# Kernel tuning notes

Hardware: AMD Instinct MI355X
Metric: run time of the kernel (lower is better)

## Reference

```python
import jax, jax.numpy as jnp
import numpy as np

N_CODES = 512
CODE_DIM = 32
BETA = 0.25


def setup_inputs() -> dict:
    key = jax.random.key(0)
    k1, k2 = jax.random.split(key)
    z_e = jax.random.normal(k1, (8192, 64, CODE_DIM), dtype=jnp.float32)
    # codebook initialized uniform in [-1/n_codes, 1/n_codes] as in the torch module
    codebook = jax.random.uniform(
        k2, (N_CODES, CODE_DIM), dtype=jnp.float32,
        minval=-1.0 / N_CODES, maxval=1.0 / N_CODES)
    return {"z_e": z_e, "codebook": codebook}


def reference(z_e, codebook):
    # squared-distance matrix: ||z||^2 - 2 z.W^T + ||W||^2  -> [B, T, n_codes]
    dists = (jnp.sum(z_e * z_e, axis=-1, keepdims=True)
             - 2.0 * jnp.einsum('btd,nd->btn', z_e, codebook)
             + jnp.sum(codebook * codebook, axis=-1))
    indices = jnp.argmin(dists, axis=-1)          # [B, T] int
    z_q = codebook[indices]                        # [B, T, code_dim]
    sg = jax.lax.stop_gradient
    codebook_loss = jnp.mean((z_q - sg(z_e)) ** 2)
    commit_loss = jnp.mean((z_e - sg(z_q)) ** 2)
    loss = codebook_loss + BETA * commit_loss
    # straight-through estimator
    z_q_st = z_e + sg(z_q - z_e)
    return (z_q_st, indices, loss)
```

## Files before the change

### kernel.cpp

```cpp
#include <hip/hip_runtime.h>

#define N_CODES 512
#define D 32
#define NVEC (8192 * 64)
#define ZQ_ELEMS (NVEC * D)
#define BT 512
#define NBLK (NVEC / BT)
#define MARGIN_TRIG 7e-5f
#define SA (-1.0f / 16.0f)
#define SB (32.0f)
#define KMASK5 0xFFFFFFE0u

typedef _Float16 half8 __attribute__((ext_vector_type(8)));
typedef float f32x4 __attribute__((ext_vector_type(4)));

#define WW1_OFF 2112
#define BFRAG_OFF 4160
#define WT_OFF 36928
#define PART_OFF 102464
#define WL_OFF 118848
#define STAGE_F4 2176

__device__ __forceinline__ unsigned umin_(unsigned a, unsigned b) { return a < b ? a : b; }
__device__ __forceinline__ unsigned umax_(unsigned a, unsigned b) { return a > b ? a : b; }

__global__ void vq_prep(const float* __restrict__ cb, float* __restrict__ ww,
                        float* __restrict__ ww1, half8* __restrict__ bfrag,
                        float* __restrict__ wT, unsigned* __restrict__ flagcnt) {
    int gid = blockIdx.x * 256 + threadIdx.x;
    if (gid == 0) *flagcnt = 0u;
    {
        int flat = gid * 4;
        int d = flat >> 9, c = flat & 511;
        float4 v;
        v.x = cb[(size_t)(c + 0) * D + d];
        v.y = cb[(size_t)(c + 1) * D + d];
        v.z = cb[(size_t)(c + 2) * D + d];
        v.w = cb[(size_t)(c + 3) * D + d];
        *(float4*)(wT + flat) = v;
    }
    if (gid < 2048) {
        int t = gid >> 6, l = gid & 63;
        int code = t * 16 + (l & 15), koff = (l >> 4) * 8;
        const float* w = cb + (size_t)code * D + koff;
        half8 h;
#pragma unroll
        for (int j = 0; j < 8; ++j) h[j] = (_Float16)(SB * w[j]);
        bfrag[t * 64 + l] = h;
    }
    if (gid < N_CODES) {
        const float* wr = cb + (size_t)gid * D;
        double s = 0.0;
#pragma unroll
        for (int d = 0; d < D; ++d) s = fma((double)wr[d], (double)wr[d], s);
        ww[gid] = (float)s;
        ww1[gid] = (float)(1.0 + s);
    }
}

__global__ __launch_bounds__(BT, 6) void vq_main(
        const float* __restrict__ z, const float* __restrict__ cbf,
        const float4* __restrict__ stage_src,
        float* __restrict__ zq, float* __restrict__ idxo,
        double* __restrict__ partials, unsigned* __restrict__ flagcnt,
        int* __restrict__ worklist, int wl_cap) {
    __shared__ __align__(16) char smem[43008];
    __shared__ double wsum[8];
    const int tid = threadIdx.x;

    {
        float4* s4 = (float4*)smem;
#pragma unroll
        for (int i = 0; i < 5; ++i) {
            int k = i * BT + tid;
            if (k < STAGE_F4) s4[k] = stage_src[k];
        }
    }
    const float* lds_cin = (const float*)smem;
    const char* lds_bf = smem + 2048;
    float4* scratch = (float4*)(smem + 34816);

    const int l = tid & 63, wv = tid >> 6;
    const int g16 = l & 15, kg = l >> 4, koff = kg * 8;
    const int vblock = blockIdx.x * BT;
    const int vwave = vblock + wv * 64;

    __syncthreads();

#pragma unroll 1
    for (int vt = 0; vt < 4; ++vt) {
        const float* zp = z + (size_t)(vwave + vt * 16 + g16) * D + koff;
        float4 a0 = *(const float4*)zp;
        float4 a1 = *(const float4*)(zp + 4);
        half8 Bz;
        Bz[0] = (_Float16)(a0.x * SA); Bz[1] = (_Float16)(a0.y * SA);
        Bz[2] = (_Float16)(a0.z * SA); Bz[3] = (_Float16)(a0.w * SA);
        Bz[4] = (_Float16)(a1.x * SA); Bz[5] = (_Float16)(a1.y * SA);
        Bz[6] = (_Float16)(a1.z * SA); Bz[7] = (_Float16)(a1.w * SA);
        float ss = 0.f;
        ss = fmaf(a0.x, a0.x, ss); ss = fmaf(a0.y, a0.y, ss);
        ss = fmaf(a0.z, a0.z, ss); ss = fmaf(a0.w, a0.w, ss);
        ss = fmaf(a1.x, a1.x, ss); ss = fmaf(a1.y, a1.y, ss);
        ss = fmaf(a1.z, a1.z, ss); ss = fmaf(a1.w, a1.w, ss);

        unsigned m1c[4], m2c[4];
#pragma unroll
        for (int r = 0; r < 4; ++r) { m1c[r] = 0xFFFFFFFFu; m2c[r] = 0xFFFFFFFFu; }

#pragma unroll
        for (int tp = 0; tp < 16; ++tp) {
            half8 W0 = *(const half8*)(lds_bf + (2 * tp) * 1024 + l * 16);
            half8 W1 = *(const half8*)(lds_bf + (2 * tp + 1) * 1024 + l * 16);
            f32x4 cv0 = *(const f32x4*)(lds_cin + (2 * tp) * 16 + kg * 4);
            f32x4 cv1 = *(const f32x4*)(lds_cin + (2 * tp + 1) * 16 + kg * 4);
            f32x4 acc0 = __builtin_amdgcn_mfma_f32_16x16x32_f16(W0, Bz, cv0, 0, 0, 0);
            f32x4 acc1 = __builtin_amdgcn_mfma_f32_16x16x32_f16(W1, Bz, cv1, 0, 0, 0);
#pragma unroll
            for (int r = 0; r < 4; ++r) {
                unsigned k0 = (__float_as_uint(acc0[r]) & KMASK5) | (unsigned)(2 * tp);
                unsigned k1 = (__float_as_uint(acc1[r]) & KMASK5) | (unsigned)(2 * tp + 1);
                unsigned med;
                asm("v_med3_u32 %0, %1, %2, %3"
                    : "=v"(med) : "v"(m1c[r]), "v"(k0), "v"(k1));
                asm("v_min3_u32 %0, %1, %2, %3"
                    : "=v"(m1c[r]) : "v"(m1c[r]), "v"(k0), "v"(k1));
                m2c[r] = umin_(m2c[r], med);
            }
        }

        unsigned a01 = umin_(m1c[0], m1c[1]), x01 = umax_(m1c[0], m1c[1]);
        unsigned a23 = umin_(m1c[2], m1c[3]), x23 = umax_(m1c[2], m1c[3]);
        unsigned b1 = umin_(a01, a23);
        unsigned sec = umin_(umax_(a01, a23), umin_(x01, x23));
        unsigned m2all = umin_(umin_(m2c[0], m2c[1]), umin_(m2c[2], m2c[3]));
        unsigned b2 = umin_(sec, m2all);
        int rwin = (m1c[0] == b1) ? 0
                 : (m1c[1] == b1) ? 1
                 : (m1c[2] == b1) ? 2 : 3;
        unsigned mymin = b1;

#pragma unroll
        for (int dd = 16; dd <= 32; dd <<= 1) {
            unsigned o1 = __shfl_xor(b1, dd, 64);
            unsigned o2 = __shfl_xor(b2, dd, 64);
            float os = __shfl_xor(ss, dd, 64);
            b2 = umin_(umin_(b2, o2), umax_(b1, o1));
            b1 = umin_(b1, o1);
            ss += os;
        }
        unsigned long long bal =
            __ballot(mymin == b1) & (0x0001000100010001ull << g16);
        int firstl = __builtin_ctzll(bal);
        int rw = __shfl(rwin, firstl, 64);
        int code = (int)(b1 & 31u) * 16 + (firstl >> 4) * 4 + rw;
        if (kg == 0)
            scratch[wv * 64 + vt * 16 + g16] =
                make_float4(__uint_as_float(b1 & KMASK5),
                            __uint_as_float(b2 & KMASK5),
                            __int_as_float(code), ss);
    }
    __syncthreads();

    float4 my = scratch[tid];
    int bai = __float_as_int(my.z);

    {
        bool flag = (my.y - my.x) <= MARGIN_TRIG;
        unsigned long long mask = __ballot(flag);
        if (mask) {
            int base = 0;
            if (l == 0) base = (int)atomicAdd(flagcnt, (unsigned)__popcll(mask));
            base = __shfl(base, 0, 64);
            if (flag) {
                int pos = base + (int)__popcll(mask & ((1ull << l) - 1ull));
                if (pos < wl_cap) worklist[pos] = vblock + tid;
            }
        }
    }

    {
        double contrib = ((double)my.x - 1.0) + (double)my.w;
#pragma unroll
        for (int off = 32; off; off >>= 1) contrib += __shfl_down(contrib, off, 64);
        if (l == 0) wsum[wv] = contrib;
    }
    __syncthreads();
    if (tid == 0) {
        double s = 0.0;
#pragma unroll
        for (int w = 0; w < 8; ++w) s += wsum[w];
        partials[blockIdx.x] = s;
    }

    idxo[vblock + tid] = (float)bai;

    {
        const float4* cb4 = (const float4*)cbf;
        float4* zq4 = (float4*)zq;
        const int c = tid & 7;
#pragma unroll
        for (int it = 0; it < 8; ++it) {
            int r = it * 64 + (tid >> 3);
            int win = __float_as_int(scratch[r].z);
            float4 val = cb4[(size_t)win * 8 + c];
            zq4[(size_t)(vblock + r) * 8 + c] = val;
        }
    }
}

__global__ __launch_bounds__(512, 2) void vq_fixup(
        const float* __restrict__ z, const float* __restrict__ cbf,
        const float* __restrict__ wT, const float* __restrict__ c32g,
        float* __restrict__ zq, float* __restrict__ idxo,
        const unsigned* __restrict__ flagcnt,
        const int* __restrict__ worklist, int wl_cap,
        const double* __restrict__ partials, float* __restrict__ loss_out) {
    __shared__ __align__(16) float wl_lds[D * N_CODES];
    __shared__ double w4[4];
    const int tid = threadIdx.x;

    {
        float4* s4 = (float4*)wl_lds;
        const float4* g4 = (const float4*)wT;
#pragma unroll
        for (int i = 0; i < 8; ++i) s4[i * 512 + tid] = g4[i * 512 + tid];
    }

    if (blockIdx.x == 0 && tid < 256) {
        double s = 0.0;
#pragma unroll
        for (int i = 0; i < NBLK / 256; ++i) s += partials[i * 256 + tid];
#pragma unroll
        for (int off = 32; off; off >>= 1) s += __shfl_down(s, off, 64);
        if ((tid & 63) == 0) w4[tid >> 6] = s;
    }
    __syncthreads();
    if (blockIdx.x == 0 && tid == 0)
        *loss_out = (float)(1.25 * (w4[0] + w4[1] + w4[2] + w4[3])
                            / (double)ZQ_ELEMS);

    int cnt = (int)*flagcnt; if (cnt > wl_cap) cnt = wl_cap;
    const int l = tid & 63;
    const int wave = (blockIdx.x * 512 + tid) >> 6;
    const int nwaves = (gridDim.x * 512) >> 6;

    for (int e = wave; e < cnt; e += nwaves) {
        int v = worklist[e];
        const float* zv = z + (size_t)v * D;
        float zd[D];
#pragma unroll
        for (int q = 0; q < 8; ++q) {
            float4 t = *(const float4*)(zv + q * 4);
            zd[4 * q + 0] = t.x; zd[4 * q + 1] = t.y;
            zd[4 * q + 2] = t.z; zd[4 * q + 3] = t.w;
        }
        double Ad = 0.0;
#pragma unroll
        for (int d = 0; d < D; ++d) Ad = fma((double)zd[d], (double)zd[d], Ad);
        float Af = (float)Ad;

        double bd[8];
#pragma unroll
        for (int k = 0; k < 8; ++k) bd[k] = 0.0;
#pragma unroll 4
        for (int d = 0; d < D; ++d) {
            double zdd = (double)zd[d];
            const float* wrow = wl_lds + d * N_CODES + l;
#pragma unroll
            for (int k = 0; k < 8; ++k)
                bd[k] = fma(zdd, (double)wrow[64 * k], bd[k]);
        }
        float best = 1e30f; int bi = 0;
#pragma unroll
        for (int k = 0; k < 8; ++k) {
            int c = l + 64 * k;
            float B32 = (float)bd[k];
            float dq = __fadd_rn(__fsub_rn(Af, __fmul_rn(2.0f, B32)), c32g[c]);
            if (dq < best) { best = dq; bi = c; }
        }
#pragma unroll
        for (int dd = 1; dd < 64; dd <<= 1) {
            float ob = __shfl_xor(best, dd, 64);
            int obi = __shfl_xor(bi, dd, 64);
            bool take = (ob < best) || (ob == best && obi < bi);
            best = take ? ob : best; bi = take ? obi : bi;
        }
        if (l == 0) idxo[v] = (float)bi;
        if (l < 8) {
            float4 val = ((const float4*)cbf)[(size_t)bi * 8 + l];
            ((float4*)zq)[(size_t)v * 8 + l] = val;
        }
    }
}

extern "C" void kernel_launch(void* const* d_in, const int* in_sizes, int n_in,
                              void* d_out, int out_size, void* d_ws, size_t ws_size,
                              hipStream_t stream) {
    const float* z  = (const float*)d_in[0];
    const float* cb = (const float*)d_in[1];
    float* out  = (float*)d_out;
    float* zq   = out;
    float* idxo = out + ZQ_ELEMS;
    float* loss = out + ZQ_ELEMS + NVEC;
    unsigned* flagcnt = (unsigned*)((char*)d_ws + 8);
    float*  ww   = (float*)((char*)d_ws + 64);
    float*  ww1  = (float*)((char*)d_ws + WW1_OFF);
    half8*  bfrag = (half8*)((char*)d_ws + BFRAG_OFF);
    float*  wT   = (float*)((char*)d_ws + WT_OFF);
    const float4* stage_src = (const float4*)((char*)d_ws + WW1_OFF);
    double* partials = (double*)((char*)d_ws + PART_OFF);
    int*    worklist = (int*)((char*)d_ws + WL_OFF);
    long long avail = (long long)ws_size - WL_OFF;
    int wl_cap = avail > 0 ? (int)(avail / 4 < NVEC ? avail / 4 : NVEC) : 0;

    vq_prep<<<16, 256, 0, stream>>>(cb, ww, ww1, bfrag, wT, flagcnt);
    vq_main<<<NBLK, BT, 0, stream>>>(z, cb, stage_src, zq, idxo,
                                     partials, flagcnt, worklist, wl_cap);
    vq_fixup<<<512, 512, 0, stream>>>(z, cb, wT, ww, zq, idxo,
                                      flagcnt, worklist, wl_cap, partials, loss);
}
```

Baseline: 119.6 us.

## Interleave four vector tiles per codebook fragment load and prefetch z before staging

Each wave now loads all four 16-vector z tiles up front, before the shared-memory staging of the codebook, so global z latency overlaps the LDS fill. The vt loop is turned inside out: each codebook fragment and bias is read from LDS once and fed to four independent MFMAs, which cuts LDS reads and gives the scheduler independent MFMA chains to interleave. Holding four tiles of running min state and accumulators raises register pressure, so the occupancy hint drops from 6 to 4 waves per SIMD.

```diff
diff --git a/kernel.cpp b/kernel.cpp
--- a/kernel.cpp
+++ b/kernel.cpp
@@ -58,7 +58,7 @@
     }
 }
 
-__global__ __launch_bounds__(BT, 6) void vq_main(
+__global__ __launch_bounds__(BT, 4) void vq_main(
         const float* __restrict__ z, const float* __restrict__ cbf,
         const float4* __restrict__ stage_src,
         float* __restrict__ zq, float* __restrict__ idxo,
@@ -67,86 +67,106 @@
     __shared__ __align__(16) char smem[43008];
     __shared__ double wsum[8];
     const int tid = threadIdx.x;
-
-    {
-        float4* s4 = (float4*)smem;
-#pragma unroll
-        for (int i = 0; i < 5; ++i) {
-            int k = i * BT + tid;
-            if (k < STAGE_F4) s4[k] = stage_src[k];
-        }
-    }
-    const float* lds_cin = (const float*)smem;
-    const char* lds_bf = smem + 2048;
-    float4* scratch = (float4*)(smem + 34816);
-
     const int l = tid & 63, wv = tid >> 6;
     const int g16 = l & 15, kg = l >> 4, koff = kg * 8;
     const int vblock = blockIdx.x * BT;
     const int vwave = vblock + wv * 64;
 
-    __syncthreads();
-
-#pragma unroll 1
+    float4 za[4][2];
+#pragma unroll
     for (int vt = 0; vt < 4; ++vt) {
         const float* zp = z + (size_t)(vwave + vt * 16 + g16) * D + koff;
-        float4 a0 = *(const float4*)zp;
-        float4 a1 = *(const float4*)(zp + 4);
-        half8 Bz;
-        Bz[0] = (_Float16)(a0.x * SA); Bz[1] = (_Float16)(a0.y * SA);
-        Bz[2] = (_Float16)(a0.z * SA); Bz[3] = (_Float16)(a0.w * SA);
-        Bz[4] = (_Float16)(a1.x * SA); Bz[5] = (_Float16)(a1.y * SA);
-        Bz[6] = (_Float16)(a1.z * SA); Bz[7] = (_Float16)(a1.w * SA);
-        float ss = 0.f;
-        ss = fmaf(a0.x, a0.x, ss); ss = fmaf(a0.y, a0.y, ss);
-        ss = fmaf(a0.z, a0.z, ss); ss = fmaf(a0.w, a0.w, ss);
-        ss = fmaf(a1.x, a1.x, ss); ss = fmaf(a1.y, a1.y, ss);
-        ss = fmaf(a1.z, a1.z, ss); ss = fmaf(a1.w, a1.w, ss);
-
-        unsigned m1c[4], m2c[4];
-#pragma unroll
-        for (int r = 0; r < 4; ++r) { m1c[r] = 0xFFFFFFFFu; m2c[r] = 0xFFFFFFFFu; }
-
-#pragma unroll
-        for (int tp = 0; tp < 16; ++tp) {
-            half8 W0 = *(const half8*)(lds_bf + (2 * tp) * 1024 + l * 16);
-            half8 W1 = *(const half8*)(lds_bf + (2 * tp + 1) * 1024 + l * 16);
-            f32x4 cv0 = *(const f32x4*)(lds_cin + (2 * tp) * 16 + kg * 4);
-            f32x4 cv1 = *(const f32x4*)(lds_cin + (2 * tp + 1) * 16 + kg * 4);
-            f32x4 acc0 = __builtin_amdgcn_mfma_f32_16x16x32_f16(W0, Bz, cv0, 0, 0, 0);
-            f32x4 acc1 = __builtin_amdgcn_mfma_f32_16x16x32_f16(W1, Bz, cv1, 0, 0, 0);
+        za[vt][0] = *(const float4*)zp;
+        za[vt][1] = *(const float4*)(zp + 4);
+    }
+
+    {
+        float4* s4 = (float4*)smem;
+#pragma unroll
+        for (int i = 0; i < 5; ++i) {
+            int k = i * BT + tid;
+            if (k < STAGE_F4) s4[k] = stage_src[k];
+        }
+    }
+    const float* lds_cin = (const float*)smem;
+    const char* lds_bf = smem + 2048;
+    float4* scratch = (float4*)(smem + 34816);
+
+    half8 Bz[4];
+    float ss[4];
+#pragma unroll
+    for (int vt = 0; vt < 4; ++vt) {
+        float4 x0 = za[vt][0], x1 = za[vt][1];
+        Bz[vt][0] = (_Float16)(x0.x * SA); Bz[vt][1] = (_Float16)(x0.y * SA);
+        Bz[vt][2] = (_Float16)(x0.z * SA); Bz[vt][3] = (_Float16)(x0.w * SA);
+        Bz[vt][4] = (_Float16)(x1.x * SA); Bz[vt][5] = (_Float16)(x1.y * SA);
+        Bz[vt][6] = (_Float16)(x1.z * SA); Bz[vt][7] = (_Float16)(x1.w * SA);
+        float s = 0.f;
+        s = fmaf(x0.x, x0.x, s); s = fmaf(x0.y, x0.y, s);
+        s = fmaf(x0.z, x0.z, s); s = fmaf(x0.w, x0.w, s);
+        s = fmaf(x1.x, x1.x, s); s = fmaf(x1.y, x1.y, s);
+        s = fmaf(x1.z, x1.z, s); s = fmaf(x1.w, x1.w, s);
+        ss[vt] = s;
+    }
+
+    __syncthreads();
+
+    unsigned m1s[4][4], m2s[4][4];
+#pragma unroll
+    for (int vt = 0; vt < 4; ++vt)
+#pragma unroll
+        for (int r = 0; r < 4; ++r) { m1s[vt][r] = 0xFFFFFFFFu; m2s[vt][r] = 0xFFFFFFFFu; }
+
+#pragma unroll
+    for (int tp = 0; tp < 16; ++tp) {
+        half8 W0 = *(const half8*)(lds_bf + (2 * tp) * 1024 + l * 16);
+        half8 W1 = *(const half8*)(lds_bf + (2 * tp + 1) * 1024 + l * 16);
+        f32x4 cv0 = *(const f32x4*)(lds_cin + (2 * tp) * 16 + kg * 4);
+        f32x4 cv1 = *(const f32x4*)(lds_cin + (2 * tp + 1) * 16 + kg * 4);
+        f32x4 acc0[4], acc1[4];
+#pragma unroll
+        for (int vt = 0; vt < 4; ++vt) {
+            acc0[vt] = __builtin_amdgcn_mfma_f32_16x16x32_f16(W0, Bz[vt], cv0, 0, 0, 0);
+            acc1[vt] = __builtin_amdgcn_mfma_f32_16x16x32_f16(W1, Bz[vt], cv1, 0, 0, 0);
+        }
+#pragma unroll
+        for (int vt = 0; vt < 4; ++vt)
 #pragma unroll
             for (int r = 0; r < 4; ++r) {
-                unsigned k0 = (__float_as_uint(acc0[r]) & KMASK5) | (unsigned)(2 * tp);
-                unsigned k1 = (__float_as_uint(acc1[r]) & KMASK5) | (unsigned)(2 * tp + 1);
+                unsigned k0 = (__float_as_uint(acc0[vt][r]) & KMASK5) | (unsigned)(2 * tp);
+                unsigned k1 = (__float_as_uint(acc1[vt][r]) & KMASK5) | (unsigned)(2 * tp + 1);
                 unsigned med;
                 asm("v_med3_u32 %0, %1, %2, %3"
-                    : "=v"(med) : "v"(m1c[r]), "v"(k0), "v"(k1));
+                    : "=v"(med) : "v"(m1s[vt][r]), "v"(k0), "v"(k1));
                 asm("v_min3_u32 %0, %1, %2, %3"
-                    : "=v"(m1c[r]) : "v"(m1c[r]), "v"(k0), "v"(k1));
-                m2c[r] = umin_(m2c[r], med);
+                    : "=v"(m1s[vt][r]) : "v"(m1s[vt][r]), "v"(k0), "v"(k1));
+                m2s[vt][r] = umin_(m2s[vt][r], med);
             }
-        }
-
-        unsigned a01 = umin_(m1c[0], m1c[1]), x01 = umax_(m1c[0], m1c[1]);
-        unsigned a23 = umin_(m1c[2], m1c[3]), x23 = umax_(m1c[2], m1c[3]);
+    }
+
+#pragma unroll
+    for (int vt = 0; vt < 4; ++vt) {
+        unsigned a01 = umin_(m1s[vt][0], m1s[vt][1]), x01 = umax_(m1s[vt][0], m1s[vt][1]);
+        unsigned a23 = umin_(m1s[vt][2], m1s[vt][3]), x23 = umax_(m1s[vt][2], m1s[vt][3]);
         unsigned b1 = umin_(a01, a23);
         unsigned sec = umin_(umax_(a01, a23), umin_(x01, x23));
-        unsigned m2all = umin_(umin_(m2c[0], m2c[1]), umin_(m2c[2], m2c[3]));
+        unsigned m2all = umin_(umin_(m2s[vt][0], m2s[vt][1]),
+                               umin_(m2s[vt][2], m2s[vt][3]));
         unsigned b2 = umin_(sec, m2all);
-        int rwin = (m1c[0] == b1) ? 0
-                 : (m1c[1] == b1) ? 1
-                 : (m1c[2] == b1) ? 2 : 3;
+        int rwin = (m1s[vt][0] == b1) ? 0
+                 : (m1s[vt][1] == b1) ? 1
+                 : (m1s[vt][2] == b1) ? 2 : 3;
         unsigned mymin = b1;
+        float ssv = ss[vt];
 
 #pragma unroll
         for (int dd = 16; dd <= 32; dd <<= 1) {
             unsigned o1 = __shfl_xor(b1, dd, 64);
             unsigned o2 = __shfl_xor(b2, dd, 64);
-            float os = __shfl_xor(ss, dd, 64);
+            float os = __shfl_xor(ssv, dd, 64);
             b2 = umin_(umin_(b2, o2), umax_(b1, o1));
             b1 = umin_(b1, o1);
-            ss += os;
+            ssv += os;
         }
         unsigned long long bal =
             __ballot(mymin == b1) & (0x0001000100010001ull << g16);
@@ -157,7 +177,7 @@
             scratch[wv * 64 + vt * 16 + g16] =
                 make_float4(__uint_as_float(b1 & KMASK5),
                             __uint_as_float(b2 & KMASK5),
-                            __int_as_float(code), ss);
+                            __int_as_float(code), ssv);
     }
     __syncthreads();
 
```

Result: slower. 184.2 us (+54.0%).
